# Kernel tuning notes

Hardware: AMD Instinct MI355X
Metric: run time of the kernel (lower is better)

## Reference

```python
import jax, jax.numpy as jnp
import numpy as np

D_MODEL = 1024
N_HEADS = 16
B, T = 4, 2048


def setup_inputs() -> dict:
    key = jax.random.key(0)
    ks = jax.random.split(key, 5)
    s_in = 1.0 / np.sqrt(D_MODEL)
    x = jax.random.normal(ks[0], (B, T, D_MODEL), dtype=jnp.float32)
    W_qkv = jax.random.uniform(ks[1], (D_MODEL, 3 * D_MODEL), jnp.float32, -s_in, s_in)
    b_qkv = jax.random.uniform(ks[2], (3 * D_MODEL,), jnp.float32, -s_in, s_in)
    W_proj = jax.random.uniform(ks[3], (D_MODEL, D_MODEL), jnp.float32, -s_in, s_in)
    b_proj = jax.random.uniform(ks[4], (D_MODEL,), jnp.float32, -s_in, s_in)
    return {"x": x, "W_qkv": W_qkv, "b_qkv": b_qkv, "W_proj": W_proj, "b_proj": b_proj}


def reference(x, W_qkv, b_qkv, W_proj, b_proj):
    b, t, c = x.shape
    hd = c // N_HEADS  # head dim
    qkv = x @ W_qkv + b_qkv                      # [B,T,3C]
    q, k, v = jnp.split(qkv, 3, axis=2)
    # [B,T,C] -> [B,H,T,hd]
    def heads(z):
        return z.reshape(b, t, N_HEADS, hd).transpose(0, 2, 1, 3)
    q, k, v = heads(q), heads(k), heads(v)
    att = jnp.einsum('bhqd,bhkd->bhqk', q, k) * (1.0 / np.sqrt(hd))
    causal = jnp.tril(jnp.ones((t, t), dtype=bool))
    att = jnp.where(causal, att, -jnp.inf)
    att = jax.nn.softmax(att, axis=-1)
    y = jnp.einsum('bhqk,bhkd->bhqd', att, v)    # [B,H,T,hd]
    y = y.transpose(0, 2, 1, 3).reshape(b, t, c)
    return y @ W_proj + b_proj
```

## Files before the change

### kernel.cpp

```cpp
#include <hip/hip_runtime.h>
#include <hip/hip_bf16.h>

typedef __attribute__((ext_vector_type(4))) float f32x4;
typedef __attribute__((ext_vector_type(8))) short s16x8;
typedef __attribute__((ext_vector_type(4))) short s16x4;

#define D_MODEL 1024
#define NH 16
#define HD 64
#define BB 4
#define TT 2048
#define MROWS (BB * TT)
#define QSCALE 0.18033688011112042f

#define MFMA16(a, b, c) __builtin_amdgcn_mfma_f32_16x16x32_bf16(a, b, c, 0, 0, 0)

#if __has_builtin(__builtin_amdgcn_mfma_f32_16x16x16_bf16)
#define PVMFMA(a, b, c) __builtin_amdgcn_mfma_f32_16x16x16_bf16(a, b, c, 0, 0, 0)
#elif __has_builtin(__builtin_amdgcn_mfma_f32_16x16x16bf16_1k)
#define PVMFMA(a, b, c) __builtin_amdgcn_mfma_f32_16x16x16bf16_1k(a, b, c, 0, 0, 0)
#else
static __device__ __forceinline__ f32x4 pv_mfma_asm(s16x4 a, s16x4 b, f32x4 c) {
  asm volatile("v_mfma_f32_16x16x16_bf16 %0, %1, %2, %0\n\ts_nop 7\n\ts_nop 7"
               : "+v"(c)
               : "v"(a), "v"(b));
  return c;
}
#define PVMFMA(a, b, c) pv_mfma_asm(a, b, c)
#endif

#define GLL16(g, l)                                                                   \
  __builtin_amdgcn_global_load_lds((const __attribute__((address_space(1))) void*)(g), \
                                   (__attribute__((address_space(3))) void*)(l), 16, 0, 0)

static __device__ __forceinline__ unsigned short f2bf(float f) {
  unsigned int u = __float_as_uint(f);
  u += 0x7fff + ((u >> 16) & 1);
  return (unsigned short)(u >> 16);
}

__global__ void k_convert(const float* __restrict__ src, short* __restrict__ dst, int n4) {
  int i = blockIdx.x * blockDim.x + threadIdx.x;
  if (i >= n4) return;
  f32x4 v = reinterpret_cast<const f32x4*>(src)[i];
  s16x4 o;
#pragma unroll
  for (int r = 0; r < 4; r++) o[r] = (short)f2bf(v[r]);
  reinterpret_cast<s16x4*>(dst)[i] = o;
}

__global__ void k_transpose(const float* __restrict__ src, short* __restrict__ dst, int K, int N) {
  __shared__ float tile[32][33];
  int n0 = blockIdx.x * 32, k0 = blockIdx.y * 32;
  int tx = threadIdx.x, ty = threadIdx.y;
#pragma unroll
  for (int i = 0; i < 4; i++) tile[ty + i * 8][tx] = src[(size_t)(k0 + ty + i * 8) * N + n0 + tx];
  __syncthreads();
#pragma unroll
  for (int i = 0; i < 4; i++)
    dst[(size_t)(n0 + ty + i * 8) * K + k0 + tx] = (short)f2bf(tile[tx][ty + i * 8]);
}

template <int MODE>
__global__ __launch_bounds__(256, 3) void k_gemm(
    const short* __restrict__ A, const short* __restrict__ Bt, const float* __restrict__ bias,
    int K, int N, short* __restrict__ outQ, short* __restrict__ outK, short* __restrict__ outV,
    float* __restrict__ outF) {
  __shared__ __align__(16) short lds_a[3][128 * 32];
  __shared__ __align__(16) short lds_b[3][128 * 32];
  const int tid = threadIdx.x;
  const int m0 = blockIdx.y * 128, n0 = blockIdx.x * 128;
  const int w = tid >> 6, lane = tid & 63;
  const int wm = (w >> 1) * 64, wn = (w & 1) * 64;
  const int lr = lane & 15, lg = lane >> 4;

  const short* aG = A + (size_t)(m0 + w * 32 + (lane >> 2)) * K + (lane & 3) * 8;
  const short* bG = Bt + (size_t)(n0 + w * 32 + (lane >> 2)) * K + (lane & 3) * 8;

#define GSTAGE(bi, kt)                                        \
  {                                                           \
    GLL16(aG + (kt), &lds_a[bi][(w * 32) * 32]);              \
    GLL16(aG + (size_t)16 * K + (kt), &lds_a[bi][(w * 32 + 16) * 32]); \
    GLL16(bG + (kt), &lds_b[bi][(w * 32) * 32]);              \
    GLL16(bG + (size_t)16 * K + (kt), &lds_b[bi][(w * 32 + 16) * 32]); \
  }

  f32x4 acc[4][4] = {};
  const int NT = K / 32;
  GSTAGE(0, 0);
  GSTAGE(1, 32);
  asm volatile("s_waitcnt vmcnt(4)" ::: "memory");
  __builtin_amdgcn_s_barrier();
  __builtin_amdgcn_sched_barrier(0);
  int cur = 0, nx2 = 2;
  for (int t = 0; t < NT; ++t) {
    if (t + 2 < NT) GSTAGE(nx2, (t + 2) * 32);
    s16x8 af[4], bfg[4];
#pragma unroll
    for (int i = 0; i < 4; i++)
      af[i] = *(const s16x8*)&lds_a[cur][(wm + i * 16 + lr) * 32 + lg * 8];
#pragma unroll
    for (int j = 0; j < 4; j++)
      bfg[j] = *(const s16x8*)&lds_b[cur][(wn + j * 16 + lr) * 32 + lg * 8];
#pragma unroll
    for (int i = 0; i < 4; i++) {
#pragma unroll
      for (int j = 0; j < 4; j++) acc[i][j] = MFMA16(af[i], bfg[j], acc[i][j]);
    }
    if (t + 2 < NT) {
      asm volatile("s_waitcnt vmcnt(4) lgkmcnt(0)" ::: "memory");
      __builtin_amdgcn_s_barrier();
      __builtin_amdgcn_sched_barrier(0);
    } else if (t + 1 < NT) {
      asm volatile("s_waitcnt vmcnt(0) lgkmcnt(0)" ::: "memory");
      __builtin_amdgcn_s_barrier();
      __builtin_amdgcn_sched_barrier(0);
    }
    cur = (cur == 2) ? 0 : cur + 1;
    nx2 = (nx2 == 2) ? 0 : nx2 + 1;
  }
#undef GSTAGE

#pragma unroll
  for (int j = 0; j < 4; j++) {
    const int ng = n0 + wn + j * 16 + lr;
    const float bv = bias[ng];
#pragma unroll
    for (int i = 0; i < 4; i++) {
      const int mg = m0 + wm + i * 16 + 4 * lg;
      if (MODE == 0) {
        const int sec = ng >> 10, c = ng & 1023, h = c >> 6, d = c & 63;
        const int b = mg >> 11, t = mg & 2047;
        const int bh = b * NH + h;
        if (sec == 2) {
          s16x4 pk;
#pragma unroll
          for (int r = 0; r < 4; r++) pk[r] = (short)f2bf(acc[i][j][r] + bv);
          *(s16x4*)&outV[((size_t)bh * HD + d) * TT + t] = pk;
        } else {
          short* dst = (sec == 0) ? outQ : outK;
          const float sc = (sec == 0) ? QSCALE : 1.0f;
#pragma unroll
          for (int r = 0; r < 4; r++)
            dst[((size_t)bh * TT + t + r) * HD + d] = (short)f2bf((acc[i][j][r] + bv) * sc);
        }
      } else {
#pragma unroll
        for (int r = 0; r < 4; r++) outF[(size_t)(mg + r) * N + ng] = acc[i][j][r] + bv;
      }
    }
  }
}

__global__ __launch_bounds__(256, 4) void k_attn(const short* __restrict__ Q,
                                                 const short* __restrict__ Kb,
                                                 const short* __restrict__ Vt,
                                                 short* __restrict__ Y) {
  __shared__ __align__(16) short kls[2][64 * 64];
  __shared__ __align__(16) short vls[2][64 * 64];
  const int tid = threadIdx.x, w = tid >> 6, lane = tid & 63;
  const int lr = lane & 15, lg = lane >> 4;
  const int bh = blockIdx.y;
  const int b = bh >> 4, h = bh & 15;
  const short* Qh = Q + (size_t)bh * TT * HD;
  const short* Kh = Kb + (size_t)bh * TT * HD;
  const short* Vh = Vt + (size_t)bh * HD * TT;
  const int srow = lane >> 3;
  const int scol = ((lane & 7) ^ srow) * 8;
  const int r7 = lr & 7;
  const s16x4 vone = {(short)0x3F80, (short)0x3F80, (short)0x3F80, (short)0x3F80};

#define STAGE(bi, kv0)                                                   \
  {                                                                      \
    const short* ks_ = Kh + (size_t)((kv0) + w * 16 + srow) * HD + scol; \
    GLL16(ks_, &kls[bi][(w * 16) * 64]);                                 \
    GLL16(ks_ + 8 * HD, &kls[bi][(w * 16 + 8) * 64]);                    \
    const short* vs_ = Vh + (size_t)(w * 16 + srow) * TT + (kv0) + scol; \
    GLL16(vs_, &vls[bi][(w * 16) * 64]);                                 \
    GLL16(vs_ + 8 * TT, &vls[bi][(w * 16 + 8) * 64]);                    \
  }

#pragma unroll
  for (int ph = 0; ph < 2; ph++) {
    const int panel = ph ? (31 - blockIdx.x) : blockIdx.x;
    const int q0w = panel * 64 + w * 16;
    s16x8 qf[2];
#pragma unroll
    for (int kc = 0; kc < 2; kc++)
      qf[kc] = *(const s16x8*)&Qh[(q0w + lr) * HD + kc * 32 + lg * 8];

    f32x4 sacc = {0.f, 0.f, 0.f, 0.f};
    f32x4 oacc[4] = {};

    const int nt = panel + 1;
    STAGE(0, 0);
    __syncthreads();
    for (int t = 0; t < nt; ++t) {
      const int cur = t & 1;
      if (t + 1 < nt) STAGE(cur ^ 1, (t + 1) * 64);
      const int kv0 = t * 64;
      s16x8 kf[4][2];
#pragma unroll
      for (int jk = 0; jk < 4; jk++)
#pragma unroll
        for (int kc = 0; kc < 2; kc++)
          kf[jk][kc] = *(const s16x8*)&kls[cur][(jk * 16 + lr) * 64 + ((kc * 4 + lg) ^ r7) * 8];
      f32x4 s[4] = {};
#pragma unroll
      for (int kc = 0; kc < 2; kc++)
#pragma unroll
        for (int jk = 0; jk < 4; jk++) s[jk] = MFMA16(kf[jk][kc], qf[kc], s[jk]);

      const bool diag = (kv0 + 63 > q0w);
      const int qg = q0w + lr;
      s16x4 pf16[4];
#pragma unroll
      for (int jk = 0; jk < 4; jk++) {
#pragma unroll
        for (int r = 0; r < 4; r++) {
          float p = exp2f(s[jk][r]);
          if (diag) {
            const int kvg = kv0 + jk * 16 + 4 * lg + r;
            p = (kvg <= qg) ? p : 0.f;
          }
          pf16[jk][r] = (short)((__float_as_uint(p) + 0x8000) >> 16);
        }
      }
#pragma unroll
      for (int jk = 0; jk < 4; jk++) {
        s16x4 vreg[4];
#pragma unroll
        for (int jd = 0; jd < 4; jd++)
          vreg[jd] = *(const s16x4*)&vls[cur][(jd * 16 + lr) * 64 +
                                              ((2 * jk + (lg >> 1)) ^ r7) * 8 + (lg & 1) * 4];
        sacc = PVMFMA(vone, pf16[jk], sacc);
#pragma unroll
        for (int jd = 0; jd < 4; jd++) oacc[jd] = PVMFMA(vreg[jd], pf16[jk], oacc[jd]);
      }
      __syncthreads();
    }
    const float inv = 1.0f / sacc[0];
    const int trow = q0w + lr;
#pragma unroll
    for (int jd = 0; jd < 4; jd++) {
      s16x4 pk;
#pragma unroll
      for (int r = 0; r < 4; r++) pk[r] = (short)f2bf(oacc[jd][r] * inv);
      *(s16x4*)&Y[((size_t)(b * TT + trow)) * D_MODEL + h * HD + jd * 16 + 4 * lg] = pk;
    }
  }
#undef STAGE
}

extern "C" void kernel_launch(void* const* d_in, const int* in_sizes, int n_in,
                              void* d_out, int out_size, void* d_ws, size_t ws_size,
                              hipStream_t stream) {
  const float* x = (const float*)d_in[0];
  const float* Wqkv = (const float*)d_in[1];
  const float* bqkv = (const float*)d_in[2];
  const float* Wproj = (const float*)d_in[3];
  const float* bproj = (const float*)d_in[4];
  float* out = (float*)d_out;

  char* ws = (char*)d_ws;
  short* Xb = (short*)ws;
  short* Wqkvt = (short*)(ws + (16u << 20));
  short* Wprojt = (short*)(ws + (22u << 20));
  short* Qb = (short*)(ws + (24u << 20));
  short* Kb = (short*)(ws + (40u << 20));
  short* Vtb = (short*)(ws + (56u << 20));
  short* Yb = Xb;

  k_convert<<<dim3(MROWS * D_MODEL / 4 / 256), 256, 0, stream>>>(x, Xb, MROWS * D_MODEL / 4);
  k_transpose<<<dim3(3 * D_MODEL / 32, D_MODEL / 32), dim3(32, 8), 0, stream>>>(
      Wqkv, Wqkvt, D_MODEL, 3 * D_MODEL);
  k_transpose<<<dim3(D_MODEL / 32, D_MODEL / 32), dim3(32, 8), 0, stream>>>(
      Wproj, Wprojt, D_MODEL, D_MODEL);
  k_gemm<0><<<dim3(3 * D_MODEL / 128, MROWS / 128), 256, 0, stream>>>(
      Xb, Wqkvt, bqkv, D_MODEL, 3 * D_MODEL, Qb, Kb, Vtb, nullptr);
  k_attn<<<dim3(16, BB * NH), 256, 0, stream>>>(Qb, Kb, Vtb, Yb);
  k_gemm<1><<<dim3(D_MODEL / 128, MROWS / 128), 256, 0, stream>>>(
      Yb, Wprojt, bproj, D_MODEL, D_MODEL, nullptr, nullptr, nullptr, out);
}
```

Baseline: 281.4 us.

## Use 256x128 tiles with XOR-swizzled 64-wide K stages for QKV GEMM; remap attention blocks per XCD

The QKV projection GEMM is split into its own kernel. It uses 512-thread blocks with a 256x128 output tile, a K step of 64 and double buffering, plus an XOR swizzle on LDS columns to avoid bank conflicts, which should give more operand reuse per global load. The attention grid is also remapped so that consecutive block IDs, which are dealt round-robin across XCDs, group blocks of the same head on the same XCD to improve L2 reuse of K and V. The cost is larger LDS use per block and a simpler two-stage pipeline that replaces the previous triple-buffered schedule.

```diff
diff --git a/kernel.cpp b/kernel.cpp
--- a/kernel.cpp
+++ b/kernel.cpp
@@ -61,11 +61,90 @@
     dst[(size_t)(n0 + ty + i * 8) * K + k0 + tx] = (short)f2bf(tile[tx][ty + i * 8]);
 }
 
-template <int MODE>
-__global__ __launch_bounds__(256, 3) void k_gemm(
+__global__ __launch_bounds__(512, 2) void k_gemm_qkv(
     const short* __restrict__ A, const short* __restrict__ Bt, const float* __restrict__ bias,
-    int K, int N, short* __restrict__ outQ, short* __restrict__ outK, short* __restrict__ outV,
+    short* __restrict__ outQ, short* __restrict__ outK, short* __restrict__ outV) {
+  const int K = D_MODEL;
+  __shared__ __align__(16) short lds_a[2][256 * 64];
+  __shared__ __align__(16) short lds_b[2][128 * 64];
+  const int tid = threadIdx.x;
+  const int m0 = blockIdx.y * 256, n0 = blockIdx.x * 128;
+  const int w = tid >> 6, lane = tid & 63;
+  const int wm = (w >> 1) * 64, wn = (w & 1) * 64;
+  const int lr = lane & 15, lg = lane >> 4;
+  const int srow = lane >> 3;
+  const int scol = ((lane & 7) ^ srow) * 8;
+  const int r7 = lr & 7;
+
+  const short* aGb = A + (size_t)(m0 + w * 32 + srow) * K + scol;
+  const short* bGb = Bt + (size_t)(n0 + w * 16 + srow) * K + scol;
+
+#define QSTAGE(bi, kt)                                                \
+  {                                                                   \
+    GLL16(aGb + (kt), &lds_a[bi][(w * 32) * 64]);                     \
+    GLL16(aGb + (size_t)8 * K + (kt), &lds_a[bi][(w * 32 + 8) * 64]); \
+    GLL16(aGb + (size_t)16 * K + (kt), &lds_a[bi][(w * 32 + 16) * 64]); \
+    GLL16(aGb + (size_t)24 * K + (kt), &lds_a[bi][(w * 32 + 24) * 64]); \
+    GLL16(bGb + (kt), &lds_b[bi][(w * 16) * 64]);                     \
+    GLL16(bGb + (size_t)8 * K + (kt), &lds_b[bi][(w * 16 + 8) * 64]); \
+  }
+
+  f32x4 acc[4][4] = {};
+  const int NT = K / 64;
+  QSTAGE(0, 0);
+  __syncthreads();
+  for (int t = 0; t < NT; ++t) {
+    const int cur = t & 1;
+    if (t + 1 < NT) QSTAGE(cur ^ 1, (t + 1) * 64);
+#pragma unroll
+    for (int ks = 0; ks < 2; ks++) {
+      s16x8 af[4], bfg[4];
+#pragma unroll
+      for (int i = 0; i < 4; i++)
+        af[i] = *(const s16x8*)&lds_a[cur][(wm + i * 16 + lr) * 64 + ((ks * 4 + lg) ^ r7) * 8];
+#pragma unroll
+      for (int j = 0; j < 4; j++)
+        bfg[j] = *(const s16x8*)&lds_b[cur][(wn + j * 16 + lr) * 64 + ((ks * 4 + lg) ^ r7) * 8];
+#pragma unroll
+      for (int i = 0; i < 4; i++) {
+#pragma unroll
+        for (int j = 0; j < 4; j++) acc[i][j] = MFMA16(af[i], bfg[j], acc[i][j]);
+      }
+    }
+    __syncthreads();
+  }
+#undef QSTAGE
+
+#pragma unroll
+  for (int j = 0; j < 4; j++) {
+    const int ng = n0 + wn + j * 16 + lr;
+    const float bv = bias[ng];
+#pragma unroll
+    for (int i = 0; i < 4; i++) {
+      const int mg = m0 + wm + i * 16 + 4 * lg;
+      const int sec = ng >> 10, c = ng & 1023, h = c >> 6, d = c & 63;
+      const int b = mg >> 11, t = mg & 2047;
+      const int bh = b * NH + h;
+      if (sec == 2) {
+        s16x4 pk;
+#pragma unroll
+        for (int r = 0; r < 4; r++) pk[r] = (short)f2bf(acc[i][j][r] + bv);
+        *(s16x4*)&outV[((size_t)bh * HD + d) * TT + t] = pk;
+      } else {
+        short* dst = (sec == 0) ? outQ : outK;
+        const float sc = (sec == 0) ? QSCALE : 1.0f;
+#pragma unroll
+        for (int r = 0; r < 4; r++)
+          dst[((size_t)bh * TT + t + r) * HD + d] = (short)f2bf((acc[i][j][r] + bv) * sc);
+      }
+    }
+  }
+}
+
+__global__ __launch_bounds__(256, 3) void k_gemm_proj(
+    const short* __restrict__ A, const short* __restrict__ Bt, const float* __restrict__ bias,
     float* __restrict__ outF) {
+  const int K = D_MODEL, N = D_MODEL;
   __shared__ __align__(16) short lds_a[3][128 * 32];
   __shared__ __align__(16) short lds_b[3][128 * 32];
   const int tid = threadIdx.x;
@@ -77,11 +156,11 @@
   const short* aG = A + (size_t)(m0 + w * 32 + (lane >> 2)) * K + (lane & 3) * 8;
   const short* bG = Bt + (size_t)(n0 + w * 32 + (lane >> 2)) * K + (lane & 3) * 8;
 
-#define GSTAGE(bi, kt)                                        \
-  {                                                           \
-    GLL16(aG + (kt), &lds_a[bi][(w * 32) * 32]);              \
+#define GSTAGE(bi, kt)                                                 \
+  {                                                                    \
+    GLL16(aG + (kt), &lds_a[bi][(w * 32) * 32]);                       \
     GLL16(aG + (size_t)16 * K + (kt), &lds_a[bi][(w * 32 + 16) * 32]); \
-    GLL16(bG + (kt), &lds_b[bi][(w * 32) * 32]);              \
+    GLL16(bG + (kt), &lds_b[bi][(w * 32) * 32]);                       \
     GLL16(bG + (size_t)16 * K + (kt), &lds_b[bi][(w * 32 + 16) * 32]); \
   }
 
@@ -128,26 +207,8 @@
 #pragma unroll
     for (int i = 0; i < 4; i++) {
       const int mg = m0 + wm + i * 16 + 4 * lg;
-      if (MODE == 0) {
-        const int sec = ng >> 10, c = ng & 1023, h = c >> 6, d = c & 63;
-        const int b = mg >> 11, t = mg & 2047;
-        const int bh = b * NH + h;
-        if (sec == 2) {
-          s16x4 pk;
-#pragma unroll
-          for (int r = 0; r < 4; r++) pk[r] = (short)f2bf(acc[i][j][r] + bv);
-          *(s16x4*)&outV[((size_t)bh * HD + d) * TT + t] = pk;
-        } else {
-          short* dst = (sec == 0) ? outQ : outK;
-          const float sc = (sec == 0) ? QSCALE : 1.0f;
-#pragma unroll
-          for (int r = 0; r < 4; r++)
-            dst[((size_t)bh * TT + t + r) * HD + d] = (short)f2bf((acc[i][j][r] + bv) * sc);
-        }
-      } else {
-#pragma unroll
-        for (int r = 0; r < 4; r++) outF[(size_t)(mg + r) * N + ng] = acc[i][j][r] + bv;
-      }
+#pragma unroll
+      for (int r = 0; r < 4; r++) outF[(size_t)(mg + r) * N + ng] = acc[i][j][r] + bv;
     }
   }
 }
@@ -160,7 +221,10 @@
   __shared__ __align__(16) short vls[2][64 * 64];
   const int tid = threadIdx.x, w = tid >> 6, lane = tid & 63;
   const int lr = lane & 15, lg = lane >> 4;
-  const int bh = blockIdx.y;
+  const int p = blockIdx.x + 16 * blockIdx.y;
+  const int xcd = p & 7, idx = p >> 3;
+  const int bh = xcd * 8 + (idx >> 4);
+  const int xq = idx & 15;
   const int b = bh >> 4, h = bh & 15;
   const short* Qh = Q + (size_t)bh * TT * HD;
   const short* Kh = Kb + (size_t)bh * TT * HD;
@@ -182,7 +246,7 @@
 
 #pragma unroll
   for (int ph = 0; ph < 2; ph++) {
-    const int panel = ph ? (31 - blockIdx.x) : blockIdx.x;
+    const int panel = ph ? (31 - xq) : xq;
     const int q0w = panel * 64 + w * 16;
     s16x8 qf[2];
 #pragma unroll
@@ -218,12 +282,12 @@
       for (int jk = 0; jk < 4; jk++) {
 #pragma unroll
         for (int r = 0; r < 4; r++) {
-          float p = exp2f(s[jk][r]);
+          float pp = exp2f(s[jk][r]);
           if (diag) {
             const int kvg = kv0 + jk * 16 + 4 * lg + r;
-            p = (kvg <= qg) ? p : 0.f;
+            pp = (kvg <= qg) ? pp : 0.f;
           }
-          pf16[jk][r] = (short)((__float_as_uint(p) + 0x8000) >> 16);
+          pf16[jk][r] = (short)((__float_as_uint(pp) + 0x8000) >> 16);
         }
       }
 #pragma unroll
@@ -276,9 +340,9 @@
       Wqkv, Wqkvt, D_MODEL, 3 * D_MODEL);
   k_transpose<<<dim3(D_MODEL / 32, D_MODEL / 32), dim3(32, 8), 0, stream>>>(
       Wproj, Wprojt, D_MODEL, D_MODEL);
-  k_gemm<0><<<dim3(3 * D_MODEL / 128, MROWS / 128), 256, 0, stream>>>(
-      Xb, Wqkvt, bqkv, D_MODEL, 3 * D_MODEL, Qb, Kb, Vtb, nullptr);
+  k_gemm_qkv<<<dim3(3 * D_MODEL / 128, MROWS / 256), 512, 0, stream>>>(
+      Xb, Wqkvt, bqkv, Qb, Kb, Vtb);
   k_attn<<<dim3(16, BB * NH), 256, 0, stream>>>(Qb, Kb, Vtb, Yb);
-  k_gemm<1><<<dim3(D_MODEL / 128, MROWS / 128), 256, 0, stream>>>(
-      Yb, Wprojt, bproj, D_MODEL, D_MODEL, nullptr, nullptr, nullptr, out);
-}
+  k_gemm_proj<<<dim3(D_MODEL / 128, MROWS / 128), 256, 0, stream>>>(
+      Yb, Wprojt, bproj, out);
+}
```

After: 289.7 us. 1.03x slower.
